# Optimization experiments

Hardware: AMD Instinct MI355X
Metric: run time of the kernel (lower is better)

Reference implementation:

```python
import jax, jax.numpy as jnp
import numpy as np

N_FILTERS = 100
WINDOWS = (2, 3, 4, 5)
B, S, W, D = 64, 400, 16, 64
VOCAB, HID = 96, 128


def setup_inputs() -> dict:
    key = jax.random.key(0)
    ks = jax.random.split(key, 16)
    inp = {
        'char_idxs': jax.random.randint(ks[0], (B, S, W), 0, VOCAB),
        'char_vectors': jax.random.normal(ks[1], (VOCAB, D), jnp.float32),
        'filt2': jax.random.normal(ks[2], (N_FILTERS, 2 * D), jnp.float32) * 0.05,
        'filt3': jax.random.normal(ks[3], (N_FILTERS, 3 * D), jnp.float32) * 0.05,
        'filt4': jax.random.normal(ks[4], (N_FILTERS, 4 * D), jnp.float32) * 0.05,
        'filt5': jax.random.normal(ks[5], (N_FILTERS, 5 * D), jnp.float32) * 0.05,
        'w_proj': jax.random.normal(ks[6], (HID, 4 * N_FILTERS), jnp.float32) * 0.05,
        't_w0': jax.random.normal(ks[7], (HID, HID), jnp.float32) * 0.05,
        't_b0': jax.random.normal(ks[8], (HID,), jnp.float32) * 0.05,
        't_w1': jax.random.normal(ks[9], (HID, HID), jnp.float32) * 0.05,
        't_b1': jax.random.normal(ks[10], (HID,), jnp.float32) * 0.05,
        'g_w0': jax.random.normal(ks[11], (HID, HID), jnp.float32) * 0.05,
        'g_b0': jax.random.normal(ks[12], (HID,), jnp.float32) * 0.05,
        'g_w1': jax.random.normal(ks[13], (HID, HID), jnp.float32) * 0.05,
        'g_b1': jax.random.normal(ks[14], (HID,), jnp.float32) * 0.05,
    }
    return inp


def _conv_branch(embed, filt, w):
    # embed: [B, S, W, D]; filt: [100, w*D]
    b, s, wl, d = embed.shape
    L = wl - w + 1  # valid positions
    idx = jnp.arange(L)[:, None] + jnp.arange(w)  # [L, w]
    xw = embed[:, :, idx, :].reshape(b, s, L, w * d)  # [B,S,L,w*D]
    h = jnp.tanh(jnp.einsum('bslk,fk->bslf', xw, filt))  # [B,S,L,100]
    return h.max(axis=2)  # max-pool over all positions -> [B,S,100]


def reference(char_idxs, char_vectors, filt2, filt3, filt4, filt5, w_proj,
              t_w0, t_b0, t_w1, t_b1, g_w0, g_b0, g_w1, g_b1):
    embed = char_vectors[char_idxs]  # [B,S,W,D]
    outs = jnp.concatenate(
        [_conv_branch(embed, f, w) for f, w in zip((filt2, filt3, filt4, filt5), WINDOWS)],
        axis=-1)  # [B,S,400]
    x = outs @ w_proj.T  # no-bias linear -> [B,S,HID]
    # 2-layer highway: x = g*relu(Wt x + bt) + (1-g)*x, g = sigmoid(Wg x + bg)
    for tw, tb, gw, gb in ((t_w0, t_b0, g_w0, g_b0), (t_w1, t_b1, g_w1, g_b1)):
        g = jax.nn.sigmoid(x @ gw.T + gb)
        t = jax.nn.relu(x @ tw.T + tb)
        x = g * t + (1.0 - g) * x
    return x
```

## Files before the change

kernel.cpp:

```cpp
#include <hip/hip_runtime.h>

#define NT     25600
#define WCH    16
#define DIM    64
#define VOCAB  96
#define HID    128
#define KP     416
#define TOKB   64
#define SLOT   9984

typedef __attribute__((ext_vector_type(8))) _Float16 h8;
typedef __attribute__((ext_vector_type(4))) float f32x4;
typedef __attribute__((ext_vector_type(4))) int i32x4;

__device__ __forceinline__ float tanh_fast(float m) {
  float t = fminf(fmaxf(m, -9.f), 9.f);
  float e = __builtin_amdgcn_exp2f(t * 2.885390082f);
  return 1.f - 2.f * __builtin_amdgcn_rcpf(e + 1.f);
}

__global__ __launch_bounds__(256) void k_prep(
    const float* __restrict__ cv,
    const float* __restrict__ f2, const float* __restrict__ f3,
    const float* __restrict__ f4, const float* __restrict__ f5,
    const float* __restrict__ wproj,
    const float* __restrict__ tw0, const float* __restrict__ gw0,
    const float* __restrict__ tw1, const float* __restrict__ gw1,
    _Float16* __restrict__ T3, _Float16* __restrict__ wprojP,
    _Float16* __restrict__ hw) {
  __shared__ float fS[100 * 65];
  __shared__ float cvS[8 * 65];
  const int tid = threadIdx.x;
  const int b = blockIdx.x;

  if (b < 168) {
    const int slot = b / 12, cg = b - slot * 12;
    int wi, j;
    if (slot < 2)      { wi = 0; j = slot; }
    else if (slot < 5) { wi = 1; j = slot - 2; }
    else if (slot < 9) { wi = 2; j = slot - 5; }
    else               { wi = 3; j = slot - 9; }
    const float* filt = (wi == 0) ? f2 : (wi == 1) ? f3 : (wi == 2) ? f4 : f5;
    const int rowlen = (wi + 2) * DIM;
    for (int idx = tid; idx < 100 * DIM; idx += 256) {
      int f = idx >> 6, d = idx & 63;
      fS[f * 65 + d] = filt[f * rowlen + j * DIM + d];
    }
    for (int idx = tid; idx < 8 * DIM; idx += 256) {
      int c = idx >> 6, d = idx & 63;
      cvS[c * 65 + d] = cv[(cg * 8 + c) * DIM + d];
    }
    __syncthreads();
    for (int idx = tid; idx < 8 * 104; idx += 256) {
      int cl = idx / 104, f = idx - cl * 104;
      float s = 0.f;
      if (f < 100) {
#pragma unroll 8
        for (int d = 0; d < DIM; ++d) s += cvS[cl * 65 + d] * fS[f * 65 + d];
      }
      T3[((size_t)slot * 96 + cg * 8 + cl) * 104 + f] = (_Float16)s;
    }
  } else if (b < 232) {
    const int n = (b - 168) * 2 + (tid >> 7);
    for (int k = tid & 127; k < KP; k += 128) {
      int s8 = k >> 3;
      int wi = s8 / 13;
      int fl = (s8 - wi * 13) * 8 + (k & 7);
      wprojP[n * KP + k] =
          (fl < 100) ? (_Float16)wproj[n * 400 + wi * 100 + fl] : (_Float16)0.f;
    }
  } else {
    const int idx = (b - 232) * 256 + tid;
    const int which = idx >> 14, r = idx & 16383;
    const float* src = (which == 0) ? tw0 : (which == 1) ? gw0
                     : (which == 2) ? tw1 : gw1;
    hw[idx] = (_Float16)src[r];
  }
}

template<int WI>
__device__ __forceinline__ void conv_block(const int* __restrict__ chars,
                                           const _Float16* __restrict__ Ts,
                                           _Float16* __restrict__ convG,
                                           int t0, int TC) {
  constexpr int W = WI + 2, L = 15 - WI;
  const int nit = TC * 13;
  for (int it = threadIdx.x; it < nit; it += 1024) {
    const int oct = it / TC, tloc = it - oct * TC;
    const int token = t0 + tloc;
    if (token >= NT) continue;
    int ch[WCH];
    {
      const i32x4* cp = (const i32x4*)(chars + (size_t)token * WCH);
#pragma unroll
      for (int q = 0; q < 4; ++q) {
        i32x4 v = cp[q];
#pragma unroll
        for (int i = 0; i < 4; ++i) ch[q * 4 + i] = v[i] * 104;
      }
    }
    const _Float16* Tb = Ts + oct * 8;
    h8 m;
    {
      h8 s = *(const h8*)(Tb + ch[0]);
#pragma unroll
      for (int j = 1; j < W; ++j) s += *(const h8*)(Tb + j * SLOT + ch[j]);
      m = s;
    }
#pragma unroll
    for (int l = 1; l < L; ++l) {
      h8 s = *(const h8*)(Tb + ch[l]);
#pragma unroll
      for (int j = 1; j < W; ++j) s += *(const h8*)(Tb + j * SLOT + ch[l + j]);
      m = __builtin_elementwise_max(m, s);
    }
    h8 r;
#pragma unroll
    for (int i = 0; i < 8; ++i) r[i] = (_Float16)tanh_fast((float)m[i]);
    const int s8 = WI * 13 + oct;
    *(h8*)(convG + ((size_t)s8 * NT + token) * 8) = r;
  }
}

__global__ __launch_bounds__(1024) void k_conv(const int* __restrict__ chars,
                                               const _Float16* __restrict__ T3,
                                               _Float16* __restrict__ convG) {
  __shared__ __align__(16) _Float16 Ts[5 * SLOT];
  const int b = blockIdx.x;
  int wi, b0, TC;
  if (b < 84)       { wi = 3; b0 = 0;   TC = 305; }
  else if (b < 156) { wi = 2; b0 = 84;  TC = 356; }
  else if (b < 214) { wi = 1; b0 = 156; TC = 442; }
  else              { wi = 0; b0 = 214; TC = 610; }
  const int W = wi + 2;
  const int SB = (wi == 0) ? 0 : (wi == 1) ? 2 : (wi == 2) ? 5 : 9;
  const int t0 = (b - b0) * TC;

  const _Float16* src = T3 + (size_t)SB * SLOT;
  const int nchunk = W * (SLOT / 8);
  for (int r = threadIdx.x; r < nchunk; r += 1024)
    *(h8*)(Ts + r * 8) = *(const h8*)(src + r * 8);
  __syncthreads();

  switch (wi) {
    case 0: conv_block<0>(chars, Ts, convG, t0, TC); break;
    case 1: conv_block<1>(chars, Ts, convG, t0, TC); break;
    case 2: conv_block<2>(chars, Ts, convG, t0, TC); break;
    default: conv_block<3>(chars, Ts, convG, t0, TC); break;
  }
}

__global__ __launch_bounds__(512) void k_head(
    const _Float16* __restrict__ convG,
    const _Float16* __restrict__ wprojP,
    const _Float16* __restrict__ hw,
    const float* __restrict__ tb0, const float* __restrict__ tb1,
    const float* __restrict__ gb0, const float* __restrict__ gb1,
    float* __restrict__ out) {
  __shared__ __align__(16) _Float16 xA[16 * 512];

  const int tid = threadIdx.x;
  const int wave = tid >> 6, lane = tid & 63;
  const int m16 = lane & 15, quad = lane >> 4;
  const int tok0 = blockIdx.x * TOKB;
  const f32x4 zero = {0.f, 0.f, 0.f, 0.f};

  const int hc = wave * 16 + m16;
  f32x4 xp[4];
#pragma unroll
  for (int mt = 0; mt < 4; ++mt) xp[mt] = zero;

  for (int ks = 0; ks < 13; ++ks) {
    const int s8 = ks * 4 + quad;
    h8 b = *(const h8*)(wprojP + (size_t)hc * KP + s8 * 8);
    const _Float16* Ag = convG + ((size_t)s8 * NT + tok0) * 8;
#pragma unroll
    for (int mt = 0; mt < 4; ++mt) {
      h8 a = *(const h8*)(Ag + (mt * 16 + m16) * 8);
      xp[mt] = __builtin_amdgcn_mfma_f32_16x16x32_f16(a, b, xp[mt], 0, 0, 0);
    }
  }

#pragma unroll
  for (int mt = 0; mt < 4; ++mt)
#pragma unroll
    for (int r = 0; r < 4; ++r)
      xA[(hc >> 3) * 512 + (mt * 16 + quad * 4 + r) * 8 + (hc & 7)] =
          (_Float16)xp[mt][r];
  __syncthreads();

#pragma unroll
  for (int layer = 0; layer < 2; ++layer) {
    const _Float16* tw = hw + (layer ? 2 : 0) * HID * HID;
    const _Float16* gw = hw + (layer ? 3 : 1) * HID * HID;
    const float* tbv = layer ? tb1 : tb0;
    const float* gbv = layer ? gb1 : gb0;
    float bt = tbv[hc], bg = gbv[hc];

    f32x4 at[4], ag[4];
#pragma unroll
    for (int mt = 0; mt < 4; ++mt) { at[mt] = zero; ag[mt] = zero; }

#pragma unroll
    for (int ks = 0; ks < 4; ++ks) {
      const int ko = ks * 32 + quad * 8;
      h8 btw = *(const h8*)(tw + (size_t)hc * HID + ko);
      h8 bgw = *(const h8*)(gw + (size_t)hc * HID + ko);
#pragma unroll
      for (int mt = 0; mt < 4; ++mt) {
        h8 a = *(const h8*)(xA + (ks * 4 + quad) * 512 + (mt * 16 + m16) * 8);
        at[mt] = __builtin_amdgcn_mfma_f32_16x16x32_f16(a, btw, at[mt], 0, 0, 0);
        ag[mt] = __builtin_amdgcn_mfma_f32_16x16x32_f16(a, bgw, ag[mt], 0, 0, 0);
      }
    }
    __syncthreads();

#pragma unroll
    for (int mt = 0; mt < 4; ++mt)
#pragma unroll
      for (int r = 0; r < 4; ++r) {
        float g = 1.f / (1.f + __builtin_amdgcn_exp2f(
                             -(ag[mt][r] + bg) * 1.442695041f));
        float tt = fmaxf(at[mt][r] + bt, 0.f);
        float xn = g * tt + (1.f - g) * xp[mt][r];
        xp[mt][r] = xn;
        int row = mt * 16 + quad * 4 + r;
        if (layer == 0)
          xA[(hc >> 3) * 512 + row * 8 + (hc & 7)] = (_Float16)xn;
        else
          out[(size_t)(tok0 + row) * HID + hc] = xn;
      }
    if (layer == 0) __syncthreads();
  }
}

template<int WI>
__device__ __forceinline__ void conv_g(const _Float16* __restrict__ T3,
                                       const int* __restrict__ ch,
                                       _Float16* __restrict__ convA,
                                       int lane, int o) {
  constexpr int W = WI + 2, L = 15 - WI;
  constexpr int SB = (WI == 0) ? 0 : (WI == 1) ? 2 : (WI == 2) ? 5 : 9;
  const _Float16* Tb = T3 + (size_t)SB * SLOT + o * 8;
  h8 m;
  {
    h8 s = *(const h8*)(Tb + ch[0]);
#pragma unroll
    for (int j = 1; j < W; ++j) s += *(const h8*)(Tb + j * SLOT + ch[j]);
    m = s;
  }
#pragma unroll
  for (int l = 1; l < L; ++l) {
    h8 s = *(const h8*)(Tb + ch[l]);
#pragma unroll
    for (int j = 1; j < W; ++j) s += *(const h8*)(Tb + j * SLOT + ch[l + j]);
    m = __builtin_elementwise_max(m, s);
  }
  h8 r;
#pragma unroll
  for (int i = 0; i < 8; ++i) r[i] = (_Float16)tanh_fast((float)m[i]);
  const int s8 = WI * 13 + o;
  *(h8*)(convA + (s8 * 64 + lane) * 8) = r;
}

__global__ __launch_bounds__(512) void k_fb(
    const int* __restrict__ chars,
    const _Float16* __restrict__ T3,
    const _Float16* __restrict__ wprojP,
    const _Float16* __restrict__ hw,
    const float* __restrict__ tb0, const float* __restrict__ tb1,
    const float* __restrict__ gb0, const float* __restrict__ gb1,
    float* __restrict__ out) {
  __shared__ __align__(16) char lds[53248];
  _Float16* convA = (_Float16*)lds;
  _Float16* xA    = (_Float16*)lds;

  const int tid = threadIdx.x;
  const int wave = tid >> 6, lane = tid & 63;
  const int m16 = lane & 15, quad = lane >> 4;
  const int tok0 = blockIdx.x * TOKB;
  const f32x4 zero = {0.f, 0.f, 0.f, 0.f};

  int ch[WCH];
  {
    const i32x4* cp = (const i32x4*)(chars + (size_t)(tok0 + lane) * WCH);
#pragma unroll
    for (int q = 0; q < 4; ++q) {
      i32x4 v = cp[q];
#pragma unroll
      for (int i = 0; i < 4; ++i) ch[q * 4 + i] = v[i] * 104;
    }
  }

  switch (wave) {
    case 0: for (int o = 0;  o < 5;  ++o) conv_g<3>(T3, ch, convA, lane, o); break;
    case 1: for (int o = 5;  o < 10; ++o) conv_g<3>(T3, ch, convA, lane, o); break;
    case 2: for (int o = 10; o < 13; ++o) conv_g<3>(T3, ch, convA, lane, o);
            for (int o = 0;  o < 2;  ++o) conv_g<2>(T3, ch, convA, lane, o); break;
    case 3: for (int o = 2;  o < 8;  ++o) conv_g<2>(T3, ch, convA, lane, o); break;
    case 4: for (int o = 8;  o < 13; ++o) conv_g<2>(T3, ch, convA, lane, o);
            conv_g<0>(T3, ch, convA, lane, 0); break;
    case 5: for (int o = 0;  o < 7;  ++o) conv_g<1>(T3, ch, convA, lane, o); break;
    case 6: for (int o = 7;  o < 13; ++o) conv_g<1>(T3, ch, convA, lane, o);
            conv_g<0>(T3, ch, convA, lane, 1); break;
    default: for (int o = 2; o < 13; ++o) conv_g<0>(T3, ch, convA, lane, o); break;
  }
  __syncthreads();

  const int hc = wave * 16 + m16;
  f32x4 xp[4];
#pragma unroll
  for (int mt = 0; mt < 4; ++mt) xp[mt] = zero;
  for (int ks = 0; ks < 13; ++ks) {
    const int s8 = ks * 4 + quad;
    h8 b = *(const h8*)(wprojP + (size_t)hc * KP + s8 * 8);
#pragma unroll
    for (int mt = 0; mt < 4; ++mt) {
      h8 a = *(const h8*)(convA + (s8 * 64 + mt * 16 + m16) * 8);
      xp[mt] = __builtin_amdgcn_mfma_f32_16x16x32_f16(a, b, xp[mt], 0, 0, 0);
    }
  }
  __syncthreads();
#pragma unroll
  for (int mt = 0; mt < 4; ++mt)
#pragma unroll
    for (int r = 0; r < 4; ++r)
      xA[(hc >> 3) * 512 + (mt * 16 + quad * 4 + r) * 8 + (hc & 7)] =
          (_Float16)xp[mt][r];
  __syncthreads();
#pragma unroll
  for (int layer = 0; layer < 2; ++layer) {
    const _Float16* tw = hw + (layer ? 2 : 0) * HID * HID;
    const _Float16* gw = hw + (layer ? 3 : 1) * HID * HID;
    const float* tbv = layer ? tb1 : tb0;
    const float* gbv = layer ? gb1 : gb0;
    float bt = tbv[hc], bg = gbv[hc];
    f32x4 at[4], ag[4];
#pragma unroll
    for (int mt = 0; mt < 4; ++mt) { at[mt] = zero; ag[mt] = zero; }
#pragma unroll
    for (int ks = 0; ks < 4; ++ks) {
      const int ko = ks * 32 + quad * 8;
      h8 btw = *(const h8*)(tw + (size_t)hc * HID + ko);
      h8 bgw = *(const h8*)(gw + (size_t)hc * HID + ko);
#pragma unroll
      for (int mt = 0; mt < 4; ++mt) {
        h8 a = *(const h8*)(xA + (ks * 4 + quad) * 512 + (mt * 16 + m16) * 8);
        at[mt] = __builtin_amdgcn_mfma_f32_16x16x32_f16(a, btw, at[mt], 0, 0, 0);
        ag[mt] = __builtin_amdgcn_mfma_f32_16x16x32_f16(a, bgw, ag[mt], 0, 0, 0);
      }
    }
    __syncthreads();
#pragma unroll
    for (int mt = 0; mt < 4; ++mt)
#pragma unroll
      for (int r = 0; r < 4; ++r) {
        float g = 1.f / (1.f + __builtin_amdgcn_exp2f(
                             -(ag[mt][r] + bg) * 1.442695041f));
        float tt = fmaxf(at[mt][r] + bt, 0.f);
        float xn = g * tt + (1.f - g) * xp[mt][r];
        xp[mt][r] = xn;
        int row = mt * 16 + quad * 4 + r;
        if (layer == 0)
          xA[(hc >> 3) * 512 + row * 8 + (hc & 7)] = (_Float16)xn;
        else
          out[(size_t)(tok0 + row) * HID + hc] = xn;
      }
    if (layer == 0) __syncthreads();
  }
}

extern "C" void kernel_launch(void* const* d_in, const int* in_sizes, int n_in,
                              void* d_out, int out_size, void* d_ws, size_t ws_size,
                              hipStream_t stream) {
  (void)in_sizes; (void)n_in; (void)out_size;
  const int* chars = (const int*)d_in[0];
  const float* cv  = (const float*)d_in[1];
  const float* f2  = (const float*)d_in[2];
  const float* f3  = (const float*)d_in[3];
  const float* f4  = (const float*)d_in[4];
  const float* f5  = (const float*)d_in[5];
  const float* wpj = (const float*)d_in[6];
  const float* tw0 = (const float*)d_in[7];
  const float* tb0 = (const float*)d_in[8];
  const float* tw1 = (const float*)d_in[9];
  const float* tb1 = (const float*)d_in[10];
  const float* gw0 = (const float*)d_in[11];
  const float* gb0 = (const float*)d_in[12];
  const float* gw1 = (const float*)d_in[13];
  const float* gb1 = (const float*)d_in[14];
  float* out = (float*)d_out;

  char* ws = (char*)d_ws;
  _Float16* T3     = (_Float16*)ws;
  _Float16* wprojP = (_Float16*)(ws + 279552);
  _Float16* hw     = (_Float16*)(ws + 386048);
  _Float16* convG  = (_Float16*)(ws + 517120);

  k_prep<<<488, 256, 0, stream>>>(cv, f2, f3, f4, f5, wpj, tw0, gw0, tw1, gw1,
                                  T3, wprojP, hw);
  if (ws_size >= (size_t)21816320) {
    k_conv<<<256, 1024, 0, stream>>>(chars, T3, convG);
    k_head<<<NT / TOKB, 512, 0, stream>>>(convG, wprojP, hw,
                                          tb0, tb1, gb0, gb1, out);
  } else {
    k_fb<<<NT / TOKB, 512, 0, stream>>>(chars, T3, wprojP, hw,
                                        tb0, tb1, gb0, gb1, out);
  }
}
```

Before: 148.1 us.

## Split conv filter octets across two blocks to halve LDS table and double grid

The conv kernel now divides the 13 filter octets of each window branch into two halves (7 and 6), each handled by a separate block with its own smaller shared-memory table, and launches 512 blocks instead of 256. The LDS footprint per block shrinks, which can allow more blocks per CU and gives more blocks across the 256 CUs. The cost is that each token's character indices are loaded twice, the table reload is a strided gather, and there are more blocks to load-balance.

```diff
diff --git a/kernel.cpp b/kernel.cpp
--- a/kernel.cpp
+++ b/kernel.cpp
@@ -78,15 +78,15 @@
   }
 }
 
-template<int WI>
+template<int WI, int OCTS>
 __device__ __forceinline__ void conv_block(const int* __restrict__ chars,
                                            const _Float16* __restrict__ Ts,
                                            _Float16* __restrict__ convG,
-                                           int t0, int TC) {
+                                           int t0, int TC, int obase) {
   constexpr int W = WI + 2, L = 15 - WI;
-  const int nit = TC * 13;
+  const int nit = TC * OCTS;
   for (int it = threadIdx.x; it < nit; it += 1024) {
-    const int oct = it / TC, tloc = it - oct * TC;
+    const int orel = it / TC, tloc = it - orel * TC;
     const int token = t0 + tloc;
     if (token >= NT) continue;
     int ch[WCH];
@@ -96,28 +96,30 @@
       for (int q = 0; q < 4; ++q) {
         i32x4 v = cp[q];
 #pragma unroll
-        for (int i = 0; i < 4; ++i) ch[q * 4 + i] = v[i] * 104;
-      }
-    }
-    const _Float16* Tb = Ts + oct * 8;
+        for (int i = 0; i < 4; ++i) ch[q * 4 + i] = v[i] * (OCTS * 8);
+      }
+    }
+    const _Float16* Tb = Ts + orel * 8;
     h8 m;
     {
       h8 s = *(const h8*)(Tb + ch[0]);
 #pragma unroll
-      for (int j = 1; j < W; ++j) s += *(const h8*)(Tb + j * SLOT + ch[j]);
+      for (int j = 1; j < W; ++j)
+        s += *(const h8*)(Tb + j * (96 * OCTS * 8) + ch[j]);
       m = s;
     }
 #pragma unroll
     for (int l = 1; l < L; ++l) {
       h8 s = *(const h8*)(Tb + ch[l]);
 #pragma unroll
-      for (int j = 1; j < W; ++j) s += *(const h8*)(Tb + j * SLOT + ch[l + j]);
+      for (int j = 1; j < W; ++j)
+        s += *(const h8*)(Tb + j * (96 * OCTS * 8) + ch[l + j]);
       m = __builtin_elementwise_max(m, s);
     }
     h8 r;
 #pragma unroll
     for (int i = 0; i < 8; ++i) r[i] = (_Float16)tanh_fast((float)m[i]);
-    const int s8 = WI * 13 + oct;
+    const int s8 = WI * 13 + obase + orel;
     *(h8*)(convG + ((size_t)s8 * NT + token) * 8) = r;
   }
 }
@@ -125,28 +127,40 @@
 __global__ __launch_bounds__(1024) void k_conv(const int* __restrict__ chars,
                                                const _Float16* __restrict__ T3,
                                                _Float16* __restrict__ convG) {
-  __shared__ __align__(16) _Float16 Ts[5 * SLOT];
+  __shared__ __align__(16) _Float16 Ts[5 * 96 * 7 * 8];
   const int b = blockIdx.x;
-  int wi, b0, TC;
-  if (b < 84)       { wi = 3; b0 = 0;   TC = 305; }
-  else if (b < 156) { wi = 2; b0 = 84;  TC = 356; }
-  else if (b < 214) { wi = 1; b0 = 156; TC = 442; }
-  else              { wi = 0; b0 = 214; TC = 610; }
+  int wi, h, b0, TC;
+  if      (b < 49)  { wi = 0; h = 0; b0 = 0;   TC = 523; }
+  else if (b < 91)  { wi = 0; h = 1; b0 = 49;  TC = 610; }
+  else if (b < 154) { wi = 1; h = 0; b0 = 91;  TC = 407; }
+  else if (b < 208) { wi = 1; h = 1; b0 = 154; TC = 475; }
+  else if (b < 285) { wi = 2; h = 0; b0 = 208; TC = 333; }
+  else if (b < 351) { wi = 2; h = 1; b0 = 285; TC = 388; }
+  else if (b < 438) { wi = 3; h = 0; b0 = 351; TC = 295; }
+  else              { wi = 3; h = 1; b0 = 438; TC = 346; }
   const int W = wi + 2;
   const int SB = (wi == 0) ? 0 : (wi == 1) ? 2 : (wi == 2) ? 5 : 9;
+  const int octs = h ? 6 : 7, obase = h ? 7 : 0;
   const int t0 = (b - b0) * TC;
 
-  const _Float16* src = T3 + (size_t)SB * SLOT;
-  const int nchunk = W * (SLOT / 8);
-  for (int r = threadIdx.x; r < nchunk; r += 1024)
-    *(h8*)(Ts + r * 8) = *(const h8*)(src + r * 8);
+  const int nch = W * 96 * octs;
+  for (int r = threadIdx.x; r < nch; r += 1024) {
+    int orel = r % octs, jc = r / octs;
+    int c = jc % 96, j = jc / 96;
+    *(h8*)(Ts + r * 8) =
+        *(const h8*)(T3 + ((size_t)(SB + j) * 96 + c) * 104 + (obase + orel) * 8);
+  }
   __syncthreads();
 
-  switch (wi) {
-    case 0: conv_block<0>(chars, Ts, convG, t0, TC); break;
-    case 1: conv_block<1>(chars, Ts, convG, t0, TC); break;
-    case 2: conv_block<2>(chars, Ts, convG, t0, TC); break;
-    default: conv_block<3>(chars, Ts, convG, t0, TC); break;
+  switch (wi * 2 + h) {
+    case 0: conv_block<0, 7>(chars, Ts, convG, t0, TC, obase); break;
+    case 1: conv_block<0, 6>(chars, Ts, convG, t0, TC, obase); break;
+    case 2: conv_block<1, 7>(chars, Ts, convG, t0, TC, obase); break;
+    case 3: conv_block<1, 6>(chars, Ts, convG, t0, TC, obase); break;
+    case 4: conv_block<2, 7>(chars, Ts, convG, t0, TC, obase); break;
+    case 5: conv_block<2, 6>(chars, Ts, convG, t0, TC, obase); break;
+    case 6: conv_block<3, 7>(chars, Ts, convG, t0, TC, obase); break;
+    default: conv_block<3, 6>(chars, Ts, convG, t0, TC, obase); break;
   }
 }
 
@@ -400,7 +414,7 @@
   k_prep<<<488, 256, 0, stream>>>(cv, f2, f3, f4, f5, wpj, tw0, gw0, tw1, gw1,
                                   T3, wprojP, hw);
   if (ws_size >= (size_t)21816320) {
-    k_conv<<<256, 1024, 0, stream>>>(chars, T3, convG);
+    k_conv<<<512, 1024, 0, stream>>>(chars, T3, convG);
     k_head<<<NT / TOKB, 512, 0, stream>>>(convG, wprojP, hw,
                                           tb0, tb1, gb0, gb1, out);
   } else {
```

Result: slower. 151.4 us (+2.2%).
